# Performance work log

Hardware: AMD Instinct MI355X
Metric: run time of the kernel (lower is better)

The kernel has to match this reference:

```python
import jax, jax.numpy as jnp
import numpy as np

V, D, DU, H = 50000, 256, 1024, 128
TEMP = 0.01

def time_cosine_emb(t, d_model):
    half = d_model // 2
    div_term = jnp.exp(jnp.arange(half, dtype=jnp.float32) * (-np.log(10000.0) / half))
    scaled = t[..., None] * div_term  # (B, L, half)
    return jnp.concatenate([jnp.sin(scaled), jnp.cos(scaled)], axis=-1)

def setup_inputs() -> dict:
    key = jax.random.key(0)
    ks = jax.random.split(key, 12)
    B, L = 64, 2048
    q_seq = jax.random.randint(ks[0], (B, L), 0, V)
    r_seq = jax.random.randint(ks[1], (B, L), 0, 3)
    t_seq = jax.random.uniform(ks[2], (B, L), dtype=jnp.float32) * 1000.0
    mask = jnp.ones((B, L), dtype=jnp.float32)
    q_tab = jax.random.normal(ks[3], (V, D), dtype=jnp.float32) * 0.02
    q_tab = q_tab.at[0].set(0.0)  # padding_idx=0
    r_tab = jax.random.normal(ks[4], (3, D), dtype=jnp.float32) * 0.02
    r_tab = r_tab.at[0].set(0.0)  # padding_idx=0
    virtual_node = jax.random.normal(ks[5], (1, D), dtype=jnp.float32)
    Ws1 = jax.random.normal(ks[6], (H, 2 * D), dtype=jnp.float32) * (1.0 / np.sqrt(2 * D))
    bs1 = jnp.zeros((H,), dtype=jnp.float32)
    Ws2 = jax.random.normal(ks[7], (1, H), dtype=jnp.float32) * (1.0 / np.sqrt(H))
    bs2 = jnp.zeros((1,), dtype=jnp.float32)
    Wa = jax.random.normal(ks[8], (DU, D), dtype=jnp.float32) * (1.0 / np.sqrt(D))
    ba = jnp.zeros((DU,), dtype=jnp.float32)
    return {"q_seq": q_seq, "r_seq": r_seq, "t_seq": t_seq, "mask": mask,
            "q_tab": q_tab, "r_tab": r_tab, "virtual_node": virtual_node,
            "Ws1": Ws1, "bs1": bs1, "Ws2": Ws2, "bs2": bs2, "Wa": Wa, "ba": ba}

def reference(q_seq, r_seq, t_seq, mask, q_tab, r_tab, virtual_node, Ws1, bs1, Ws2, bs2, Wa, ba):
    B, L = q_seq.shape
    d_model = q_tab.shape[1]
    # embedding gathers + trig time embedding
    h_events = q_tab[q_seq] + r_tab[r_seq] + time_cosine_emb(t_seq, d_model)  # (B,L,D)
    h_virtual = jnp.broadcast_to(virtual_node[None, :, :], (B, L, d_model))
    pair = jnp.concatenate([h_events, h_virtual], axis=-1)  # (B,L,2D)
    # struct_head: Linear -> LeakyReLU(0.2) -> Linear
    hdn = jax.nn.leaky_relu(jnp.einsum('bld,hd->blh', pair, Ws1) + bs1, 0.2)
    logits = jnp.einsum('blh,oh->blo', hdn, Ws2) + bs2  # (B,L,1)
    A_hat = jax.nn.sigmoid(logits / TEMP) * mask[..., None]
    # aggregator: Linear -> LeakyReLU(0.2)
    h_trans = jax.nn.leaky_relu(jnp.einsum('bld,ud->blu', h_events, Wa) + ba, 0.2)  # (B,L,DU)
    u_i = jnp.sum(h_trans * A_hat, axis=1)  # (B,DU)
    return (u_i, jnp.squeeze(A_hat, -1))
```

## Files before the change

kernel.cpp:

```cpp
#include <hip/hip_runtime.h>

typedef unsigned short ushort_t;
typedef unsigned int uint_t;

typedef short bf16x8 __attribute__((ext_vector_type(8)));
typedef float f32x4 __attribute__((ext_vector_type(4)));

#define MFMA16(a, b, c) __builtin_amdgcn_mfma_f32_16x16x32_bf16(a, b, c, 0, 0, 0)

__device__ __forceinline__ ushort_t f2bf(float f) {
    uint_t u = __float_as_uint(f);
    u += 0x7fffu + ((u >> 16) & 1u);
    return (ushort_t)(u >> 16);
}
__device__ __forceinline__ float bf2f(ushort_t h) {
    return __uint_as_float(((uint_t)h) << 16);
}

__device__ __forceinline__ void async16(const ushort_t* g, ushort_t* l) {
    __builtin_amdgcn_global_load_lds(
        (const __attribute__((address_space(1))) uint_t*)g,
        (__attribute__((address_space(3))) uint_t*)l, 16, 0, 0);
}

__global__ void k_prep(const float* __restrict__ Ws1, const float* __restrict__ bs1,
                       const float* __restrict__ virt, const float* __restrict__ Wa,
                       float* __restrict__ consth, ushort_t* __restrict__ wa_b,
                       ushort_t* __restrict__ ws1h, ushort_t* __restrict__ ws1l) {
    int b = blockIdx.x;
    if (b == 0) {
        int h = threadIdx.x;
        if (h < 128) {
            const float* row = Ws1 + h * 512 + 256;
            float s = bs1[h];
            for (int d = 0; d < 256; ++d) s += row[d] * virt[d];
            consth[h] = s;
        }
        return;
    }
    const float* src;
    int src_stride, tid;
    ushort_t *dhi, *dlo;
    if (b <= 128) {
        tid = (b - 1) * 256 + threadIdx.x;
        src = Wa; src_stride = 256; dhi = wa_b; dlo = nullptr;
    } else {
        tid = (b - 129) * 256 + threadIdx.x;
        src = Ws1; src_stride = 512; dhi = ws1h; dlo = ws1l;
    }
    int pl = tid & 15, kc = (tid >> 4) & 31, pt = tid >> 9;
    int row = pt * 16 + pl;
    const float* s = src + (size_t)row * src_stride + kc * 8;
    ushort_t hs[8], ls[8];
#pragma unroll
    for (int j = 0; j < 8; ++j) {
        float v = s[j];
        ushort_t h = f2bf(v);
        hs[j] = h;
        ls[j] = f2bf(v - bf2f(h));
    }
    uint4 hv;
    hv.x = hs[0] | ((uint_t)hs[1] << 16); hv.y = hs[2] | ((uint_t)hs[3] << 16);
    hv.z = hs[4] | ((uint_t)hs[5] << 16); hv.w = hs[6] | ((uint_t)hs[7] << 16);
    *(uint4*)(dhi + (size_t)tid * 8) = hv;
    if (dlo) {
        uint4 lv;
        lv.x = ls[0] | ((uint_t)ls[1] << 16); lv.y = ls[2] | ((uint_t)ls[3] << 16);
        lv.z = ls[4] | ((uint_t)ls[5] << 16); lv.w = ls[6] | ((uint_t)ls[7] << 16);
        *(uint4*)(dlo + (size_t)tid * 8) = lv;
    }
}

__global__ __launch_bounds__(256, 2) void k_embed_struct(
    const int* __restrict__ q_seq, const int* __restrict__ r_seq,
    const float* __restrict__ t_seq, const float* __restrict__ q_tab,
    const float* __restrict__ r_tab,
    const ushort_t* __restrict__ ws1h, const ushort_t* __restrict__ ws1l,
    const float* __restrict__ consth, const float* __restrict__ Ws2,
    const float* __restrict__ bs2, const float* __restrict__ mask,
    ushort_t* __restrict__ h_hi, float* __restrict__ out_ahat) {
    __shared__ __align__(16) char region[66560];
    __shared__ float sdiv[128];
    __shared__ float sLogit[64];
    ushort_t* sQ = (ushort_t*)region;
    ushort_t* sAhi = (ushort_t*)region;
    ushort_t* sAlo = (ushort_t*)(region + 32768);
    int tid = threadIdx.x;
    if (tid < 128) sdiv[tid] = __expf((float)tid * -0.07195578415606394f);
    if (tid < 64) sLogit[tid] = 0.0f;
    int w = tid >> 6, lane = tid & 63;
    int pl = lane & 15, kq = lane >> 4;
    int nl = pl;
    int p0 = blockIdx.x * 64;
    int p = p0 + w * 16 + pl;
    int qv = q_seq[p0 + w * 16 + pl];
    int rr = r_seq[p];
    float tt = t_seq[p];
#pragma unroll
    for (int i = 0; i < 16; ++i) {
        int row = __shfl(qv, i, 64);
        async16((const ushort_t*)(q_tab + (size_t)row * 256) + lane * 8,
                sQ + (w * 16 + i) * 520);
    }
    __syncthreads();
    uint4 hvA[8], lvA[8];
    const char* myrow = (const char*)sQ + (w * 16 + pl) * 1040;
    const float* rrow = r_tab + (size_t)rr * 256;
#pragma unroll
    for (int it = 0; it < 8; ++it) {
        int kc = it * 4 + kq;
        int k0 = kc * 8;
        float4 qa = *(const float4*)(myrow + kc * 32);
        float4 qb = *(const float4*)(myrow + kc * 32 + 16);
        float4 ra = *(const float4*)(rrow + kc * 8);
        float4 rb = *(const float4*)(rrow + kc * 8 + 4);
        float v[8] = {qa.x + ra.x, qa.y + ra.y, qa.z + ra.z, qa.w + ra.w,
                      qb.x + rb.x, qb.y + rb.y, qb.z + rb.z, qb.w + rb.w};
        bool iscos = (kc >= 16);
#pragma unroll
        for (int j = 0; j < 8; ++j) {
            float ang = tt * sdiv[(k0 + j) & 127];
            v[j] += iscos ? __cosf(ang) : __sinf(ang);
        }
        ushort_t hs[8], ls[8];
#pragma unroll
        for (int j = 0; j < 8; ++j) {
            ushort_t h = f2bf(v[j]);
            hs[j] = h;
            ls[j] = f2bf(v[j] - bf2f(h));
        }
        uint4 hv, lv;
        hv.x = hs[0] | ((uint_t)hs[1] << 16); hv.y = hs[2] | ((uint_t)hs[3] << 16);
        hv.z = hs[4] | ((uint_t)hs[5] << 16); hv.w = hs[6] | ((uint_t)hs[7] << 16);
        lv.x = ls[0] | ((uint_t)ls[1] << 16); lv.y = ls[2] | ((uint_t)ls[3] << 16);
        lv.z = ls[4] | ((uint_t)ls[5] << 16); lv.w = ls[6] | ((uint_t)ls[7] << 16);
        hvA[it] = hv; lvA[it] = lv;
        *(uint4*)(h_hi + ((size_t)((blockIdx.x * 4 + w) * 32 + kc) * 16 + pl) * 8) = hv;
    }
    __syncthreads();
#pragma unroll
    for (int it = 0; it < 8; ++it) {
        int kc = it * 4 + kq;
        int loff = ((w * 32 + kc) * 16 + pl) * 8;
        *(uint4*)(sAhi + loff) = hvA[it];
        *(uint4*)(sAlo + loff) = lvA[it];
    }
    __syncthreads();
    f32x4 acc[4][2];
    f32x4 z4 = {0.f, 0.f, 0.f, 0.f};
#pragma unroll
    for (int mt = 0; mt < 4; ++mt)
#pragma unroll
        for (int nt = 0; nt < 2; ++nt) acc[mt][nt] = z4;
    bf16x8 bhi[2], blo[2], nbhi[2], nblo[2];
#pragma unroll
    for (int nt = 0; nt < 2; ++nt) {
        int off = (((w * 2 + nt) * 32 + kq) * 16 + nl) * 8;
        bhi[nt] = *(const bf16x8*)(ws1h + off);
        blo[nt] = *(const bf16x8*)(ws1l + off);
    }
#pragma unroll 1
    for (int ks = 0; ks < 8; ++ks) {
        if (ks < 7) {
#pragma unroll
            for (int nt = 0; nt < 2; ++nt) {
                int off = (((w * 2 + nt) * 32 + (ks + 1) * 4 + kq) * 16 + nl) * 8;
                nbhi[nt] = *(const bf16x8*)(ws1h + off);
                nblo[nt] = *(const bf16x8*)(ws1l + off);
            }
        }
        bf16x8 ahi[4], alo[4];
#pragma unroll
        for (int mt = 0; mt < 4; ++mt) {
            int off = ((mt * 32 + ks * 4 + kq) * 16 + nl) * 8;
            ahi[mt] = *(const bf16x8*)&sAhi[off];
            alo[mt] = *(const bf16x8*)&sAlo[off];
        }
#pragma unroll
        for (int mt = 0; mt < 4; ++mt)
#pragma unroll
            for (int nt = 0; nt < 2; ++nt) {
                acc[mt][nt] = MFMA16(ahi[mt], bhi[nt], acc[mt][nt]);
                acc[mt][nt] = MFMA16(alo[mt], bhi[nt], acc[mt][nt]);
                acc[mt][nt] = MFMA16(ahi[mt], blo[nt], acc[mt][nt]);
            }
#pragma unroll
        for (int nt = 0; nt < 2; ++nt) { bhi[nt] = nbhi[nt]; blo[nt] = nblo[nt]; }
    }
    float ps[4][4];
#pragma unroll
    for (int mt = 0; mt < 4; ++mt)
#pragma unroll
        for (int r = 0; r < 4; ++r) ps[mt][r] = 0.f;
#pragma unroll
    for (int nt = 0; nt < 2; ++nt) {
        int ng = w * 32 + nt * 16 + nl;
        float chv = consth[ng], w2 = Ws2[ng];
#pragma unroll
        for (int mt = 0; mt < 4; ++mt)
#pragma unroll
            for (int r = 0; r < 4; ++r) {
                float v = acc[mt][nt][r] + chv;
                v = v > 0.f ? v : 0.2f * v;
                ps[mt][r] += v * w2;
            }
    }
#pragma unroll
    for (int mt = 0; mt < 4; ++mt)
#pragma unroll
        for (int r = 0; r < 4; ++r) {
            float x = ps[mt][r];
            x += __shfl_xor(x, 1, 64);
            x += __shfl_xor(x, 2, 64);
            x += __shfl_xor(x, 4, 64);
            x += __shfl_xor(x, 8, 64);
            ps[mt][r] = x;
        }
    if (nl == 0) {
#pragma unroll
        for (int mt = 0; mt < 4; ++mt)
#pragma unroll
            for (int r = 0; r < 4; ++r)
                atomicAdd(&sLogit[mt * 16 + kq * 4 + r], ps[mt][r]);
    }
    __syncthreads();
    if (tid < 64) {
        int pp = p0 + tid;
        float lg = sLogit[tid] + bs2[0];
        float y = lg * 100.0f;
        y = fminf(fmaxf(y, -60.f), 60.f);
        float a = 1.0f / (1.0f + expf(-y));
        out_ahat[pp] = a * mask[pp];
    }
}

__global__ __launch_bounds__(256, 2) void k_agg(
    const ushort_t* __restrict__ h_hi, const ushort_t* __restrict__ wa_blk,
    const float* __restrict__ ba, const float* __restrict__ ahat,
    float* __restrict__ u_i) {
    __shared__ ushort_t sB[2][16384];
    __shared__ float sAh[128];
    int tid = threadIdx.x;
    int w = tid >> 6, lane = tid & 63, nl = lane & 15, kq = lane >> 4;
    int p0 = blockIdx.x * 128, bidx = p0 >> 11;
    if (tid < 128) sAh[tid] = ahat[p0 + tid];
    int mh = w & 1, nh = w >> 1;
    bf16x8 afr[4][8];
    const ushort_t* gA = h_hi + (size_t)(p0 >> 4) * 4096;
#pragma unroll
    for (int mt = 0; mt < 4; ++mt) {
        const ushort_t* base = gA + (size_t)(mh * 4 + mt) * 4096;
#pragma unroll
        for (int ks = 0; ks < 8; ++ks)
            afr[mt][ks] = *(const bf16x8*)(base + ks * 512 + lane * 8);
    }
#define STAGE_HALF(buf, nch_, kh_)                                              \
    {                                                                           \
        int t0 = w * 2;                                                         \
        _Pragma("unroll")                                                       \
        for (int tt = 0; tt < 2; ++tt) {                                        \
            int t = t0 + tt;                                                    \
            const ushort_t* src =                                               \
                wa_blk + (size_t)((nch_) * 8 + t) * 4096 + (kh_) * 2048;        \
            _Pragma("unroll")                                                   \
            for (int c = 0; c < 4; ++c)                                         \
                async16(src + c * 512 + lane * 8, &sB[buf][t * 2048 + c * 512]);\
        }                                                                       \
    }
    f32x4 acc[4][4];
    f32x4 z4 = {0.f, 0.f, 0.f, 0.f};
#pragma unroll
    for (int mt = 0; mt < 4; ++mt)
#pragma unroll
        for (int nt = 0; nt < 4; ++nt) acc[mt][nt] = z4;
    STAGE_HALF(0, 0, 0);
    __syncthreads();
#pragma unroll 1
    for (int nch = 0; nch < 8; ++nch) {
        STAGE_HALF(1, nch, 1);
#pragma unroll
        for (int ksl = 0; ksl < 4; ++ksl) {
            bf16x8 bfr[4];
#pragma unroll
            for (int nt = 0; nt < 4; ++nt)
                bfr[nt] = *(const bf16x8*)&sB[0][(nh * 4 + nt) * 2048 + (ksl * 4 + kq) * 128 + nl * 8];
#pragma unroll
            for (int mt = 0; mt < 4; ++mt)
#pragma unroll
                for (int nt = 0; nt < 4; ++nt)
                    acc[mt][nt] = MFMA16(afr[mt][ksl], bfr[nt], acc[mt][nt]);
        }
        __syncthreads();
        if (nch < 7) STAGE_HALF(0, nch + 1, 0);
#pragma unroll
        for (int ksl = 0; ksl < 4; ++ksl) {
            bf16x8 bfr[4];
#pragma unroll
            for (int nt = 0; nt < 4; ++nt)
                bfr[nt] = *(const bf16x8*)&sB[1][(nh * 4 + nt) * 2048 + (ksl * 4 + kq) * 128 + nl * 8];
#pragma unroll
            for (int mt = 0; mt < 4; ++mt)
#pragma unroll
                for (int nt = 0; nt < 4; ++nt)
                    acc[mt][nt] = MFMA16(afr[mt][4 + ksl], bfr[nt], acc[mt][nt]);
        }
        __syncthreads();
        int n0 = nch * 128;
#pragma unroll
        for (int nt = 0; nt < 4; ++nt) {
            int ng = n0 + nh * 64 + nt * 16 + nl;
            float ban = ba[ng];
            float s = 0.f;
#pragma unroll
            for (int mt = 0; mt < 4; ++mt)
#pragma unroll
                for (int r = 0; r < 4; ++r) {
                    float v = acc[mt][nt][r] + ban;
                    v = v > 0.f ? v : 0.2f * v;
                    int ml = mh * 64 + mt * 16 + kq * 4 + r;
                    s += v * sAh[ml];
                    acc[mt][nt][r] = 0.f;
                }
            s += __shfl_xor(s, 16, 64);
            s += __shfl_xor(s, 32, 64);
            if (kq == 0) atomicAdd(&u_i[bidx * 1024 + ng], s);
        }
    }
#undef STAGE_HALF
}

extern "C" void kernel_launch(void* const* d_in, const int* in_sizes, int n_in,
                              void* d_out, int out_size, void* d_ws, size_t ws_size,
                              hipStream_t stream) {
    const int* q_seq = (const int*)d_in[0];
    const int* r_seq = (const int*)d_in[1];
    const float* t_seq = (const float*)d_in[2];
    const float* mask = (const float*)d_in[3];
    const float* q_tab = (const float*)d_in[4];
    const float* r_tab = (const float*)d_in[5];
    const float* virt = (const float*)d_in[6];
    const float* Ws1 = (const float*)d_in[7];
    const float* bs1 = (const float*)d_in[8];
    const float* Ws2 = (const float*)d_in[9];
    const float* bs2 = (const float*)d_in[10];
    const float* Wa = (const float*)d_in[11];
    const float* ba = (const float*)d_in[12];
    float* out = (float*)d_out;

    ushort_t* h_hi = (ushort_t*)d_ws;
    ushort_t* wa_b = h_hi + 33554432;
    ushort_t* ws1h = wa_b + 262144;
    ushort_t* ws1l = ws1h + 32768;
    float* ch = (float*)(ws1l + 32768);

    hipMemsetAsync(out, 0, 65536 * sizeof(float), stream);
    hipLaunchKernelGGL(k_prep, dim3(145), dim3(256), 0, stream,
                       Ws1, bs1, virt, Wa, ch, wa_b, ws1h, ws1l);
    hipLaunchKernelGGL(k_embed_struct, dim3(2048), dim3(256), 0, stream,
                       q_seq, r_seq, t_seq, q_tab, r_tab, ws1h, ws1l, ch, Ws2, bs2,
                       mask, h_hi, out + 65536);
    hipLaunchKernelGGL(k_agg, dim3(1024), dim3(256), 0, stream,
                       h_hi, wa_b, ba, out + 65536, out);
}
```

Measured before the change: 259.3 us.

## Load Wa fragments directly from global into registers, dropping LDS staging

The aggregator kernel stops staging Wa tiles through double-buffered shared memory with async global-to-LDS copies and block barriers. Each wave now reads its B fragments straight from global memory into registers, prefetching one k-step ahead, and the first MFMA uses a zero accumulator instead of an explicit reset. This removes the LDS traffic, LDS footprint and per-chunk syncthreads, but each pair of waves now fetches the same Wa data separately, and load latency is hidden only by the one-step register prefetch.

```diff
diff --git a/kernel.cpp b/kernel.cpp
--- a/kernel.cpp
+++ b/kernel.cpp
@@ -238,7 +238,6 @@
     const ushort_t* __restrict__ h_hi, const ushort_t* __restrict__ wa_blk,
     const float* __restrict__ ba, const float* __restrict__ ahat,
     float* __restrict__ u_i) {
-    __shared__ ushort_t sB[2][16384];
     __shared__ float sAh[128];
     int tid = threadIdx.x;
     int w = tid >> 6, lane = tid & 63, nl = lane & 15, kq = lane >> 4;
@@ -254,57 +253,40 @@
         for (int ks = 0; ks < 8; ++ks)
             afr[mt][ks] = *(const bf16x8*)(base + ks * 512 + lane * 8);
     }
-#define STAGE_HALF(buf, nch_, kh_)                                              \
-    {                                                                           \
-        int t0 = w * 2;                                                         \
-        _Pragma("unroll")                                                       \
-        for (int tt = 0; tt < 2; ++tt) {                                        \
-            int t = t0 + tt;                                                    \
-            const ushort_t* src =                                               \
-                wa_blk + (size_t)((nch_) * 8 + t) * 4096 + (kh_) * 2048;        \
-            _Pragma("unroll")                                                   \
-            for (int c = 0; c < 4; ++c)                                         \
-                async16(src + c * 512 + lane * 8, &sB[buf][t * 2048 + c * 512]);\
-        }                                                                       \
-    }
-    f32x4 acc[4][4];
-    f32x4 z4 = {0.f, 0.f, 0.f, 0.f};
-#pragma unroll
-    for (int mt = 0; mt < 4; ++mt)
-#pragma unroll
-        for (int nt = 0; nt < 4; ++nt) acc[mt][nt] = z4;
-    STAGE_HALF(0, 0, 0);
-    __syncthreads();
+    __syncthreads();
+    const ushort_t* gBw = wa_blk + (size_t)nh * 4 * 4096 + lane * 8;
 #pragma unroll 1
     for (int nch = 0; nch < 8; ++nch) {
-        STAGE_HALF(1, nch, 1);
-#pragma unroll
-        for (int ksl = 0; ksl < 4; ++ksl) {
-            bf16x8 bfr[4];
-#pragma unroll
-            for (int nt = 0; nt < 4; ++nt)
-                bfr[nt] = *(const bf16x8*)&sB[0][(nh * 4 + nt) * 2048 + (ksl * 4 + kq) * 128 + nl * 8];
-#pragma unroll
-            for (int mt = 0; mt < 4; ++mt)
+        const ushort_t* gB = gBw + (size_t)nch * 32768;
+        f32x4 acc[4][4];
+        bf16x8 bcur[4], bnxt[4];
+#pragma unroll
+        for (int nt = 0; nt < 4; ++nt)
+            bcur[nt] = *(const bf16x8*)(gB + nt * 4096);
+#pragma unroll
+        for (int ks = 0; ks < 8; ++ks) {
+            if (ks < 7) {
 #pragma unroll
                 for (int nt = 0; nt < 4; ++nt)
-                    acc[mt][nt] = MFMA16(afr[mt][ksl], bfr[nt], acc[mt][nt]);
-        }
-        __syncthreads();
-        if (nch < 7) STAGE_HALF(0, nch + 1, 0);
-#pragma unroll
-        for (int ksl = 0; ksl < 4; ++ksl) {
-            bf16x8 bfr[4];
-#pragma unroll
-            for (int nt = 0; nt < 4; ++nt)
-                bfr[nt] = *(const bf16x8*)&sB[1][(nh * 4 + nt) * 2048 + (ksl * 4 + kq) * 128 + nl * 8];
-#pragma unroll
-            for (int mt = 0; mt < 4; ++mt)
-#pragma unroll
-                for (int nt = 0; nt < 4; ++nt)
-                    acc[mt][nt] = MFMA16(afr[mt][4 + ksl], bfr[nt], acc[mt][nt]);
-        }
-        __syncthreads();
+                    bnxt[nt] = *(const bf16x8*)(gB + nt * 4096 + (ks + 1) * 512);
+            }
+            if (ks == 0) {
+                f32x4 z4 = {0.f, 0.f, 0.f, 0.f};
+#pragma unroll
+                for (int mt = 0; mt < 4; ++mt)
+#pragma unroll
+                    for (int nt = 0; nt < 4; ++nt)
+                        acc[mt][nt] = MFMA16(afr[mt][0], bcur[nt], z4);
+            } else {
+#pragma unroll
+                for (int mt = 0; mt < 4; ++mt)
+#pragma unroll
+                    for (int nt = 0; nt < 4; ++nt)
+                        acc[mt][nt] = MFMA16(afr[mt][ks], bcur[nt], acc[mt][nt]);
+            }
+#pragma unroll
+            for (int nt = 0; nt < 4; ++nt) bcur[nt] = bnxt[nt];
+        }
         int n0 = nch * 128;
 #pragma unroll
         for (int nt = 0; nt < 4; ++nt) {
@@ -319,14 +301,12 @@
                     v = v > 0.f ? v : 0.2f * v;
                     int ml = mh * 64 + mt * 16 + kq * 4 + r;
                     s += v * sAh[ml];
-                    acc[mt][nt][r] = 0.f;
                 }
             s += __shfl_xor(s, 16, 64);
             s += __shfl_xor(s, 32, 64);
             if (kq == 0) atomicAdd(&u_i[bidx * 1024 + ng], s);
         }
     }
-#undef STAGE_HALF
 }
 
 extern "C" void kernel_launch(void* const* d_in, const int* in_sizes, int n_in,
```

After: 263.0 us. No clear change (+1.4%).
